# Performance work log

Measured on AMD Instinct MI355X. Metric: run time of the kernel, lower is better.

## Reference

```python
import jax, jax.numpy as jnp
import numpy as np

COMMITMENT_COST = 0.25


def setup_inputs() -> dict:
    key = jax.random.key(0)
    k1, k2 = jax.random.split(key)
    inputs = jax.random.normal(k1, (256, 512, 64), dtype=jnp.float32)
    embedding = jax.random.normal(k2, (1024, 64), dtype=jnp.float32) * 4.0
    return {"inputs": inputs, "embedding": embedding}


def reference(inputs, embedding):
    # inputs: [B, T, D], embedding: [K, D]
    input_shape = inputs.shape
    D = embedding.shape[-1]
    flat = inputs.reshape(-1, D)  # [N, D]
    # squared-L2 distances: [N, K]
    distances = (
        jnp.sum(flat * flat, axis=1, keepdims=True)
        + jnp.sum(embedding * embedding, axis=1)[None, :]
        - 2.0 * flat @ embedding.T
    )
    encoding_indices = jnp.argmin(distances, axis=1)  # [N]
    # one-hot @ embedding == gather
    quantized = embedding[encoding_indices].reshape(input_shape)  # [B, T, D]
    # squared-L2 commitment / codebook loss
    e_latent_loss = jnp.sum((jax.lax.stop_gradient(quantized) - inputs) ** 2, axis=-1)
    q_latent_loss = jnp.sum((quantized - jax.lax.stop_gradient(inputs)) ** 2, axis=-1)
    quantization_loss = q_latent_loss + COMMITMENT_COST * e_latent_loss  # [B, T]
    # straight-through estimator
    quantized_sg = inputs + jax.lax.stop_gradient(quantized - inputs)
    encoding_indices = encoding_indices.reshape(input_shape[:-1])  # [B, T]
    return quantized_sg, encoding_indices, quantization_loss
```

## Files before the change

### kernel.cpp

```cpp
#include <hip/hip_runtime.h>
#include <hip/hip_bf16.h>

#define D 64
#define KCODES 1024
#define MARGIN 0.25f
#define FLAG_CAP 8192

typedef __attribute__((ext_vector_type(8))) short bf16x8;
typedef __attribute__((ext_vector_type(4))) float f32x4;

__device__ inline unsigned short f2bf(float f) {
    union { __hip_bfloat16 h; unsigned short s; } cv;
    cv.h = __float2bfloat16(f);
    return cv.s;
}
__device__ inline float bf2f(unsigned short v) {
    union { unsigned short s; __hip_bfloat16 h; } cv;
    cv.s = v;
    return __bfloat162float(cv.h);
}

__global__ __launch_bounds__(256) void prep_kernel(
    const float* __restrict__ emb, float* __restrict__ e2,
    unsigned short* __restrict__ ehi, unsigned short* __restrict__ elo,
    unsigned int* __restrict__ counter) {
    int t = blockIdx.x * 256 + threadIdx.x;
    if (t == 0) *counter = 0u;
    if (t < KCODES) {
        const float4* ep = (const float4*)(emb + (size_t)t * D);
        float s0 = 0.f, s1 = 0.f, s2 = 0.f, s3 = 0.f;
#pragma unroll
        for (int i = 0; i < 16; ++i) {
            float4 v = ep[i];
            s0 = fmaf(v.x, v.x, s0);
            s1 = fmaf(v.y, v.y, s1);
            s2 = fmaf(v.z, v.z, s2);
            s3 = fmaf(v.w, v.w, s3);
        }
        e2[t] = (s0 + s1) + (s2 + s3);
    }
    float v = emb[t];
    unsigned short h = f2bf(v);
    ehi[t] = h;
    elo[t] = f2bf(v - bf2f(h));
}

__global__ __launch_bounds__(256) void vq_mfma_kernel(
    const float* __restrict__ x, const float* __restrict__ emb,
    const float* __restrict__ e2, const unsigned short* __restrict__ ehi,
    const unsigned short* __restrict__ elo, float* __restrict__ out_q,
    float* __restrict__ out_idx, float* __restrict__ out_loss,
    unsigned int* __restrict__ counter, int* __restrict__ flaglist) {
    __shared__ int s_bi[256];
    const int tid = threadIdx.x;
    const int lane = tid & 63;
    const int wave = __builtin_amdgcn_readfirstlane(tid >> 6);
    const int quad = lane >> 4;
    const int l15 = lane & 15;
    const int rowBase = blockIdx.x * 256 + wave * 64;

    bf16x8 ah[4][2], al[4][2];
#pragma unroll
    for (int rs = 0; rs < 4; ++rs) {
        const float* xr = x + (size_t)(rowBase + rs * 16 + l15) * D;
#pragma unroll
        for (int c = 0; c < 2; ++c) {
            const float4* p = (const float4*)(xr + c * 32 + quad * 8);
            float4 f0 = p[0], f1 = p[1];
            float f[8] = {f0.x, f0.y, f0.z, f0.w, f1.x, f1.y, f1.z, f1.w};
            bf16x8 h, l;
#pragma unroll
            for (int j = 0; j < 8; ++j) {
                unsigned short hu = f2bf(f[j]);
                h[j] = (short)hu;
                l[j] = (short)f2bf(f[j] - bf2f(hu));
            }
            ah[rs][c] = h;
            al[rs][c] = l;
        }
    }

    float m1[4][4], m2[4][4];
    int i1[4][4];
#pragma unroll
    for (int rs = 0; rs < 4; ++rs)
#pragma unroll
        for (int r = 0; r < 4; ++r) {
            m1[rs][r] = 3.4e38f;
            m2[rs][r] = 3.4e38f;
            i1[rs][r] = 0;
        }

    for (int t = 0; t < 64; ++t) {
        const int code = t * 16 + l15;
        const float e2v = e2[code];
        const unsigned short* hb = ehi + (size_t)code * D + quad * 8;
        const unsigned short* lb = elo + (size_t)code * D + quad * 8;
        bf16x8 bh0 = *(const bf16x8*)(hb);
        bf16x8 bh1 = *(const bf16x8*)(hb + 32);
        bf16x8 bl0 = *(const bf16x8*)(lb);
        bf16x8 bl1 = *(const bf16x8*)(lb + 32);
#pragma unroll
        for (int rs = 0; rs < 4; ++rs) {
            f32x4 acc = {0.f, 0.f, 0.f, 0.f};
            acc = __builtin_amdgcn_mfma_f32_16x16x32_bf16(ah[rs][0], bh0, acc, 0, 0, 0);
            acc = __builtin_amdgcn_mfma_f32_16x16x32_bf16(ah[rs][0], bl0, acc, 0, 0, 0);
            acc = __builtin_amdgcn_mfma_f32_16x16x32_bf16(al[rs][0], bh0, acc, 0, 0, 0);
            acc = __builtin_amdgcn_mfma_f32_16x16x32_bf16(ah[rs][1], bh1, acc, 0, 0, 0);
            acc = __builtin_amdgcn_mfma_f32_16x16x32_bf16(ah[rs][1], bl1, acc, 0, 0, 0);
            acc = __builtin_amdgcn_mfma_f32_16x16x32_bf16(al[rs][1], bh1, acc, 0, 0, 0);
#pragma unroll
            for (int r = 0; r < 4; ++r) {
                float v = fmaf(-2.0f, acc[r], e2v);
                if (v < m1[rs][r]) {
                    m2[rs][r] = m1[rs][r];
                    m1[rs][r] = v;
                    i1[rs][r] = code;
                } else {
                    m2[rs][r] = fminf(m2[rs][r], v);
                }
            }
        }
    }

#pragma unroll
    for (int rs = 0; rs < 4; ++rs)
#pragma unroll
        for (int r = 0; r < 4; ++r) {
            float v1 = m1[rs][r], v2 = m2[rs][r];
            int ix = i1[rs][r];
#pragma unroll
            for (int mask = 1; mask < 16; mask <<= 1) {
                float o1 = __shfl_xor(v1, mask);
                int oi = __shfl_xor(ix, mask);
                float o2 = __shfl_xor(v2, mask);
                v2 = fminf(fminf(v2, o2), fmaxf(v1, o1));
                bool take = (o1 < v1) || (o1 == v1 && oi < ix);
                v1 = take ? o1 : v1;
                ix = take ? oi : ix;
            }
            m1[rs][r] = v1;
            m2[rs][r] = v2;
            i1[rs][r] = ix;
        }

    if (l15 == 0) {
#pragma unroll
        for (int rs = 0; rs < 4; ++rs)
#pragma unroll
            for (int r = 0; r < 4; ++r) {
                int lrow = wave * 64 + rs * 16 + quad * 4 + r;
                s_bi[lrow] = i1[rs][r];
                if (m2[rs][r] - m1[rs][r] < MARGIN) {
                    unsigned int slot = atomicAdd(counter, 1u);
                    if (slot < FLAG_CAP) flaglist[slot] = blockIdx.x * 256 + lrow;
                }
            }
    }
    __syncthreads();

    {
        const int row = blockIdx.x * 256 + tid;
        const int bi = s_bi[tid];
        const float4* qp = (const float4*)(emb + (size_t)bi * D);
        const float4* xp = (const float4*)(x + (size_t)row * D);
        float4* oq = (float4*)(out_q + (size_t)row * D);
        float l0 = 0.f, l1 = 0.f, l2 = 0.f, l3 = 0.f;
#pragma unroll
        for (int i = 0; i < 16; ++i) {
            float4 q = qp[i];
            float4 xv = xp[i];
            float a0 = q.x - xv.x, a1 = q.y - xv.y, a2 = q.z - xv.z, a3 = q.w - xv.w;
            l0 = fmaf(a0, a0, l0);
            l1 = fmaf(a1, a1, l1);
            l2 = fmaf(a2, a2, l2);
            l3 = fmaf(a3, a3, l3);
            float4 o;
            o.x = xv.x + a0;
            o.y = xv.y + a1;
            o.z = xv.z + a2;
            o.w = xv.w + a3;
            oq[i] = o;
        }
        float s = (l0 + l1) + (l2 + l3);
        out_idx[row] = (float)bi;
        out_loss[row] = s + 0.25f * s;
    }
}

__global__ __launch_bounds__(256) void rescore_kernel(
    const float* __restrict__ x, const float* __restrict__ emb,
    const float* __restrict__ e2, float* __restrict__ out_q,
    float* __restrict__ out_idx, float* __restrict__ out_loss,
    const unsigned int* __restrict__ counter, const int* __restrict__ flaglist) {
    __shared__ float s_d[256];
    __shared__ int s_i[256];
    __shared__ float s_a[D];
    unsigned int n = *counter;
    if (n > FLAG_CAP) n = FLAG_CAP;
    const int tid = threadIdx.x;
    for (unsigned int f = blockIdx.x; f < n; f += gridDim.x) {
        const int row = flaglist[f];
        const float* xr = x + (size_t)row * D;
        float xv[D];
        const float4* xp = (const float4*)xr;
#pragma unroll
        for (int i = 0; i < 16; ++i) {
            float4 v = xp[i];
            xv[4 * i + 0] = v.x;
            xv[4 * i + 1] = v.y;
            xv[4 * i + 2] = v.z;
            xv[4 * i + 3] = v.w;
        }
        float bd = 3.4e38f;
        int bi = 0;
        for (int kk = 0; kk < 4; ++kk) {
            const int k = tid + kk * 256;
            const float* ek = emb + (size_t)k * D;
            float d0 = 0.f, d1 = 0.f, d2 = 0.f, d3 = 0.f;
#pragma unroll
            for (int i = 0; i < 16; ++i) {
                d0 = fmaf(xv[4 * i + 0], ek[4 * i + 0], d0);
                d1 = fmaf(xv[4 * i + 1], ek[4 * i + 1], d1);
                d2 = fmaf(xv[4 * i + 2], ek[4 * i + 2], d2);
                d3 = fmaf(xv[4 * i + 3], ek[4 * i + 3], d3);
            }
            float dist = fmaf(-2.0f, (d0 + d1) + (d2 + d3), e2[k]);
            if (dist < bd) { bd = dist; bi = k; }
        }
        s_d[tid] = bd;
        s_i[tid] = bi;
        __syncthreads();
        for (int s = 128; s > 0; s >>= 1) {
            if (tid < s) {
                float od = s_d[tid + s];
                int oi = s_i[tid + s];
                if (od < s_d[tid] || (od == s_d[tid] && oi < s_i[tid])) {
                    s_d[tid] = od;
                    s_i[tid] = oi;
                }
            }
            __syncthreads();
        }
        const int fbi = s_i[0];
        if (tid < D) {
            float xe = xr[tid];
            float a = emb[(size_t)fbi * D + tid] - xe;
            out_q[(size_t)row * D + tid] = xe + a;
            s_a[tid] = a * a;
        }
        __syncthreads();
        if (tid == 0) {
            float l0 = 0.f, l1 = 0.f, l2 = 0.f, l3 = 0.f;
            for (int i = 0; i < 16; ++i) {
                l0 += s_a[4 * i + 0];
                l1 += s_a[4 * i + 1];
                l2 += s_a[4 * i + 2];
                l3 += s_a[4 * i + 3];
            }
            float s = (l0 + l1) + (l2 + l3);
            out_loss[row] = s + 0.25f * s;
            out_idx[row] = (float)fbi;
        }
        __syncthreads();
    }
}

extern "C" void kernel_launch(void* const* d_in, const int* in_sizes, int n_in,
                              void* d_out, int out_size, void* d_ws, size_t ws_size,
                              hipStream_t stream) {
    const float* x = (const float*)d_in[0];
    const float* emb = (const float*)d_in[1];
    const int nrows = in_sizes[0] / D;

    float* out_q = (float*)d_out;
    float* out_idx = out_q + (size_t)nrows * D;
    float* out_loss = out_idx + nrows;

    char* ws = (char*)d_ws;
    float* e2 = (float*)ws;
    unsigned short* ehi = (unsigned short*)(ws + 4096);
    unsigned short* elo = (unsigned short*)(ws + 4096 + 131072);
    unsigned int* counter = (unsigned int*)(ws + 4096 + 2 * 131072);
    int* flaglist = (int*)(ws + 4096 + 2 * 131072 + 64);

    prep_kernel<<<(KCODES * D) / 256, 256, 0, stream>>>(emb, e2, ehi, elo, counter);
    vq_mfma_kernel<<<nrows / 256, 256, 0, stream>>>(x, emb, e2, ehi, elo, out_q,
                                                    out_idx, out_loss, counter,
                                                    flaglist);
    rescore_kernel<<<256, 256, 0, stream>>>(x, emb, e2, out_q, out_idx, out_loss,
                                            counter, flaglist);
}
```

Before: 195.1 us.

## Stage codebook through double-buffered LDS, pack argmin keys, batch rescore rows

The main kernel now handles 128 rows per block and stages the bf16 hi/lo codebook tiles through a double-buffered, XOR-swizzled LDS ring with explicit prefetch. It folds -2x into the bf16 split inputs and seeds the accumulator with an offset e2 so distances stay positive. That lets it pack the tile index into the low mantissa bits and track top-2 with v_med3_u32 and integer min. The rescore kernel processes 8 flagged rows per block, reusing each codebook load across them, and the flag capacity is derived from workspace size. Truncating mantissa bits and widening the margin to 0.6 trades argmin precision for fewer compare instructions but more rows sent to the rescore pass.

New measurement: 265.9 us. +36.3%, slower.

```diff
diff --git a/kernel.cpp b/kernel.cpp
--- a/kernel.cpp
+++ b/kernel.cpp
@@ -3,25 +3,25 @@
 
 #define D 64
 #define KCODES 1024
-#define MARGIN 0.25f
-#define FLAG_CAP 8192
+#define MARGIN 0.6f
+#define OFFSET 2048.0f
 
 typedef __attribute__((ext_vector_type(8))) short bf16x8;
 typedef __attribute__((ext_vector_type(4))) float f32x4;
 
-__device__ inline unsigned short f2bf(float f) {
+__device__ __forceinline__ unsigned short f2bf(float f) {
     union { __hip_bfloat16 h; unsigned short s; } cv;
     cv.h = __float2bfloat16(f);
     return cv.s;
 }
-__device__ inline float bf2f(unsigned short v) {
+__device__ __forceinline__ float bf2f(unsigned short v) {
     union { unsigned short s; __hip_bfloat16 h; } cv;
     cv.s = v;
     return __bfloat162float(cv.h);
 }
 
 __global__ __launch_bounds__(256) void prep_kernel(
-    const float* __restrict__ emb, float* __restrict__ e2,
+    const float* __restrict__ emb, float* __restrict__ e2, float* __restrict__ e2b,
     unsigned short* __restrict__ ehi, unsigned short* __restrict__ elo,
     unsigned int* __restrict__ counter) {
     int t = blockIdx.x * 256 + threadIdx.x;
@@ -37,7 +37,9 @@
             s2 = fmaf(v.z, v.z, s2);
             s3 = fmaf(v.w, v.w, s3);
         }
-        e2[t] = (s0 + s1) + (s2 + s3);
+        float s = (s0 + s1) + (s2 + s3);
+        e2[t] = s;
+        e2b[t] = s + OFFSET;
     }
     float v = emb[t];
     unsigned short h = f2bf(v);
@@ -45,23 +47,25 @@
     elo[t] = f2bf(v - bf2f(h));
 }
 
-__global__ __launch_bounds__(256) void vq_mfma_kernel(
+__global__ __launch_bounds__(256, 4) void vq_mfma_kernel(
     const float* __restrict__ x, const float* __restrict__ emb,
-    const float* __restrict__ e2, const unsigned short* __restrict__ ehi,
+    const float* __restrict__ e2b, const unsigned short* __restrict__ ehi,
     const unsigned short* __restrict__ elo, float* __restrict__ out_q,
     float* __restrict__ out_idx, float* __restrict__ out_loss,
-    unsigned int* __restrict__ counter, int* __restrict__ flaglist) {
-    __shared__ int s_bi[256];
+    unsigned int* __restrict__ counter, int* __restrict__ flaglist, int flag_cap) {
+    __shared__ float4 lds4[2][256];
+    __shared__ int s_bi[128];
+    char* ldsc = (char*)&lds4[0][0];
     const int tid = threadIdx.x;
     const int lane = tid & 63;
     const int wave = __builtin_amdgcn_readfirstlane(tid >> 6);
     const int quad = lane >> 4;
     const int l15 = lane & 15;
-    const int rowBase = blockIdx.x * 256 + wave * 64;
-
-    bf16x8 ah[4][2], al[4][2];
-#pragma unroll
-    for (int rs = 0; rs < 4; ++rs) {
+    const int rowBase = blockIdx.x * 128 + wave * 32;
+
+    bf16x8 ah[2][2], al[2][2];
+#pragma unroll
+    for (int rs = 0; rs < 2; ++rs) {
         const float* xr = x + (size_t)(rowBase + rs * 16 + l15) * D;
 #pragma unroll
         for (int c = 0; c < 2; ++c) {
@@ -71,96 +75,127 @@
             bf16x8 h, l;
 #pragma unroll
             for (int j = 0; j < 8; ++j) {
-                unsigned short hu = f2bf(f[j]);
+                float v = -2.0f * f[j];
+                unsigned short hu = f2bf(v);
                 h[j] = (short)hu;
-                l[j] = (short)f2bf(f[j] - bf2f(hu));
+                l[j] = (short)f2bf(v - bf2f(hu));
             }
             ah[rs][c] = h;
             al[rs][c] = l;
         }
     }
 
-    float m1[4][4], m2[4][4];
-    int i1[4][4];
-#pragma unroll
-    for (int rs = 0; rs < 4; ++rs)
+    const int r3 = lane >> 3;
+    const int sl = lane & 7;
+    const int halfsel = wave & 1;
+    const unsigned short* sbase = (wave < 2) ? ehi : elo;
+    const unsigned short* gsrc0 = sbase + halfsel * 512 + lane * 8;
+    const int wrow = halfsel * 8 + r3;
+    char* wdst = ldsc + ((wave < 2) ? 0 : 2048) + wrow * 128 + ((sl ^ r3) << 4);
+
+    const int s7 = l15 & 7;
+    const int rdA = l15 * 128 + ((quad ^ s7) << 4);
+    const int rdB = l15 * 128 + (((quad + 4) ^ s7) << 4);
+
+    unsigned int m1[2][4], m2[2][4];
+#pragma unroll
+    for (int rs = 0; rs < 2; ++rs)
+#pragma unroll
+        for (int r = 0; r < 4; ++r) { m1[rs][r] = 0xFFFFFFFFu; m2[rs][r] = 0xFFFFFFFFu; }
+
+    auto compute = [&](int t, float e2v, bf16x8 bh0, bf16x8 bh1, bf16x8 bl0, bf16x8 bl1) {
+        f32x4 cvec = {e2v, e2v, e2v, e2v};
+        unsigned tt = (unsigned)t;
+#pragma unroll
+        for (int rs = 0; rs < 2; ++rs) {
+            f32x4 acc = cvec;
+            acc = __builtin_amdgcn_mfma_f32_16x16x32_bf16(ah[rs][0], bh0, acc, 0, 0, 0);
+            acc = __builtin_amdgcn_mfma_f32_16x16x32_bf16(al[rs][0], bh0, acc, 0, 0, 0);
+            acc = __builtin_amdgcn_mfma_f32_16x16x32_bf16(ah[rs][0], bl0, acc, 0, 0, 0);
+            acc = __builtin_amdgcn_mfma_f32_16x16x32_bf16(ah[rs][1], bh1, acc, 0, 0, 0);
+            acc = __builtin_amdgcn_mfma_f32_16x16x32_bf16(al[rs][1], bh1, acc, 0, 0, 0);
+            acc = __builtin_amdgcn_mfma_f32_16x16x32_bf16(ah[rs][1], bl1, acc, 0, 0, 0);
+#pragma unroll
+            for (int r = 0; r < 4; ++r) {
+                unsigned k = (__float_as_uint(acc[r]) & 0xFFFFFFC0u) | tt;
+                unsigned nm2;
+                asm("v_med3_u32 %0, %1, %2, %3"
+                    : "=v"(nm2)
+                    : "v"(m1[rs][r]), "v"(m2[rs][r]), "v"(k));
+                m2[rs][r] = nm2;
+                m1[rs][r] = (k < m1[rs][r]) ? k : m1[rs][r];
+            }
+        }
+    };
+
+    float e2cur = e2b[l15];
+    {
+        float4 stg = *(const float4*)gsrc0;
+        *(float4*)wdst = stg;
+    }
+    __syncthreads();
+
+#pragma unroll 1
+    for (int i = 0; i < 32; ++i) {
+        const int tB = 2 * i + 1;
+        float4 stgB = *(const float4*)(gsrc0 + (size_t)tB * 1024);
+        float e2nA = e2b[tB * 16 + l15];
+        {
+            bf16x8 bh0 = *(const bf16x8*)(ldsc + rdA);
+            bf16x8 bh1 = *(const bf16x8*)(ldsc + rdB);
+            bf16x8 bl0 = *(const bf16x8*)(ldsc + 2048 + rdA);
+            bf16x8 bl1 = *(const bf16x8*)(ldsc + 2048 + rdB);
+            compute(2 * i, e2cur, bh0, bh1, bl0, bl1);
+        }
+        *(float4*)(wdst + 4096) = stgB;
+        __syncthreads();
+        float4 stgA2 = *(const float4*)(gsrc0 + (size_t)(tB + 1) * 1024);
+        float e2nB = e2b[(tB + 1) * 16 + l15];
+        {
+            bf16x8 bh0 = *(const bf16x8*)(ldsc + 4096 + rdA);
+            bf16x8 bh1 = *(const bf16x8*)(ldsc + 4096 + rdB);
+            bf16x8 bl0 = *(const bf16x8*)(ldsc + 6144 + rdA);
+            bf16x8 bl1 = *(const bf16x8*)(ldsc + 6144 + rdB);
+            compute(tB, e2nA, bh0, bh1, bl0, bl1);
+        }
+        *(float4*)wdst = stgA2;
+        __syncthreads();
+        e2cur = e2nB;
+    }
+
+#pragma unroll
+    for (int rs = 0; rs < 2; ++rs)
 #pragma unroll
         for (int r = 0; r < 4; ++r) {
-            m1[rs][r] = 3.4e38f;
-            m2[rs][r] = 3.4e38f;
-            i1[rs][r] = 0;
-        }
-
-    for (int t = 0; t < 64; ++t) {
-        const int code = t * 16 + l15;
-        const float e2v = e2[code];
-        const unsigned short* hb = ehi + (size_t)code * D + quad * 8;
-        const unsigned short* lb = elo + (size_t)code * D + quad * 8;
-        bf16x8 bh0 = *(const bf16x8*)(hb);
-        bf16x8 bh1 = *(const bf16x8*)(hb + 32);
-        bf16x8 bl0 = *(const bf16x8*)(lb);
-        bf16x8 bl1 = *(const bf16x8*)(lb + 32);
-#pragma unroll
-        for (int rs = 0; rs < 4; ++rs) {
-            f32x4 acc = {0.f, 0.f, 0.f, 0.f};
-            acc = __builtin_amdgcn_mfma_f32_16x16x32_bf16(ah[rs][0], bh0, acc, 0, 0, 0);
-            acc = __builtin_amdgcn_mfma_f32_16x16x32_bf16(ah[rs][0], bl0, acc, 0, 0, 0);
-            acc = __builtin_amdgcn_mfma_f32_16x16x32_bf16(al[rs][0], bh0, acc, 0, 0, 0);
-            acc = __builtin_amdgcn_mfma_f32_16x16x32_bf16(ah[rs][1], bh1, acc, 0, 0, 0);
-            acc = __builtin_amdgcn_mfma_f32_16x16x32_bf16(ah[rs][1], bl1, acc, 0, 0, 0);
-            acc = __builtin_amdgcn_mfma_f32_16x16x32_bf16(al[rs][1], bh1, acc, 0, 0, 0);
-#pragma unroll
-            for (int r = 0; r < 4; ++r) {
-                float v = fmaf(-2.0f, acc[r], e2v);
-                if (v < m1[rs][r]) {
-                    m2[rs][r] = m1[rs][r];
-                    m1[rs][r] = v;
-                    i1[rs][r] = code;
-                } else {
-                    m2[rs][r] = fminf(m2[rs][r], v);
+            unsigned v1 = m1[rs][r], v2 = m2[rs][r];
+            const unsigned my1 = v1;
+#pragma unroll
+            for (int mask = 1; mask < 16; mask <<= 1) {
+                unsigned o1 = __shfl_xor(v1, mask);
+                unsigned o2 = __shfl_xor(v2, mask);
+                unsigned hi = v1 > o1 ? v1 : o1;
+                unsigned lo2 = v2 < o2 ? v2 : o2;
+                v2 = lo2 < hi ? lo2 : hi;
+                v1 = v1 < o1 ? v1 : o1;
+            }
+            unsigned long long bal = __ballot(my1 == v1);
+            int winl = __ffsll((bal >> (quad * 16)) & 0xFFFFull) - 1;
+            int code = (int)(v1 & 63u) * 16 + winl;
+            if (l15 == 0) {
+                int lrow = wave * 32 + rs * 16 + quad * 4 + r;
+                s_bi[lrow] = code;
+                float f1 = __uint_as_float(v1 & 0xFFFFFFC0u);
+                float f2 = __uint_as_float(v2 & 0xFFFFFFC0u);
+                if (f2 - f1 < MARGIN) {
+                    unsigned slot = atomicAdd(counter, 1u);
+                    if (slot < (unsigned)flag_cap) flaglist[slot] = blockIdx.x * 128 + lrow;
                 }
             }
         }
-    }
-
-#pragma unroll
-    for (int rs = 0; rs < 4; ++rs)
-#pragma unroll
-        for (int r = 0; r < 4; ++r) {
-            float v1 = m1[rs][r], v2 = m2[rs][r];
-            int ix = i1[rs][r];
-#pragma unroll
-            for (int mask = 1; mask < 16; mask <<= 1) {
-                float o1 = __shfl_xor(v1, mask);
-                int oi = __shfl_xor(ix, mask);
-                float o2 = __shfl_xor(v2, mask);
-                v2 = fminf(fminf(v2, o2), fmaxf(v1, o1));
-                bool take = (o1 < v1) || (o1 == v1 && oi < ix);
-                v1 = take ? o1 : v1;
-                ix = take ? oi : ix;
-            }
-            m1[rs][r] = v1;
-            m2[rs][r] = v2;
-            i1[rs][r] = ix;
-        }
-
-    if (l15 == 0) {
-#pragma unroll
-        for (int rs = 0; rs < 4; ++rs)
-#pragma unroll
-            for (int r = 0; r < 4; ++r) {
-                int lrow = wave * 64 + rs * 16 + quad * 4 + r;
-                s_bi[lrow] = i1[rs][r];
-                if (m2[rs][r] - m1[rs][r] < MARGIN) {
-                    unsigned int slot = atomicAdd(counter, 1u);
-                    if (slot < FLAG_CAP) flaglist[slot] = blockIdx.x * 256 + lrow;
-                }
-            }
-    }
     __syncthreads();
 
-    {
-        const int row = blockIdx.x * 256 + tid;
+    if (tid < 128) {
+        const int row = blockIdx.x * 128 + tid;
         const int bi = s_bi[tid];
         const float4* qp = (const float4*)(emb + (size_t)bi * D);
         const float4* xp = (const float4*)(x + (size_t)row * D);
@@ -192,77 +227,113 @@
     const float* __restrict__ x, const float* __restrict__ emb,
     const float* __restrict__ e2, float* __restrict__ out_q,
     float* __restrict__ out_idx, float* __restrict__ out_loss,
-    const unsigned int* __restrict__ counter, const int* __restrict__ flaglist) {
-    __shared__ float s_d[256];
-    __shared__ int s_i[256];
-    __shared__ float s_a[D];
+    const unsigned int* __restrict__ counter, const int* __restrict__ flaglist,
+    int flag_cap) {
+    __shared__ float s_x[8][64];
+    __shared__ int s_rows[8];
+    __shared__ float s_wd[8][4];
+    __shared__ int s_wi[8][4];
+    __shared__ float s_a[4][64];
     unsigned int n = *counter;
-    if (n > FLAG_CAP) n = FLAG_CAP;
+    if (n > (unsigned)flag_cap) n = (unsigned)flag_cap;
     const int tid = threadIdx.x;
-    for (unsigned int f = blockIdx.x; f < n; f += gridDim.x) {
-        const int row = flaglist[f];
-        const float* xr = x + (size_t)row * D;
-        float xv[D];
-        const float4* xp = (const float4*)xr;
-#pragma unroll
-        for (int i = 0; i < 16; ++i) {
-            float4 v = xp[i];
-            xv[4 * i + 0] = v.x;
-            xv[4 * i + 1] = v.y;
-            xv[4 * i + 2] = v.z;
-            xv[4 * i + 3] = v.w;
-        }
-        float bd = 3.4e38f;
-        int bi = 0;
+    const int lane = tid & 63;
+    const int wv = tid >> 6;
+    for (unsigned int b = blockIdx.x; b * 8u < n; b += gridDim.x) {
+        const unsigned base = b * 8u;
+        unsigned nbu = n - base;
+        if (nbu > 8u) nbu = 8u;
+        const int nb = (int)nbu;
+        if (tid < 8) s_rows[tid] = flaglist[base + (tid < nb ? tid : 0)];
+        __syncthreads();
+        if (tid < 128) {
+            int r = tid >> 4, q4 = tid & 15;
+            ((float4*)&s_x[r][0])[q4] = ((const float4*)(x + (size_t)s_rows[r] * D))[q4];
+        }
+        __syncthreads();
+
+        float bd_[8];
+        int bi_[8];
+#pragma unroll
+        for (int r = 0; r < 8; ++r) { bd_[r] = 3.4e38f; bi_[r] = 0; }
         for (int kk = 0; kk < 4; ++kk) {
             const int k = tid + kk * 256;
             const float* ek = emb + (size_t)k * D;
-            float d0 = 0.f, d1 = 0.f, d2 = 0.f, d3 = 0.f;
+            float d0[8], d1[8], d2[8], d3[8];
+#pragma unroll
+            for (int r = 0; r < 8; ++r) { d0[r] = 0.f; d1[r] = 0.f; d2[r] = 0.f; d3[r] = 0.f; }
 #pragma unroll
             for (int i = 0; i < 16; ++i) {
-                d0 = fmaf(xv[4 * i + 0], ek[4 * i + 0], d0);
-                d1 = fmaf(xv[4 * i + 1], ek[4 * i + 1], d1);
-                d2 = fmaf(xv[4 * i + 2], ek[4 * i + 2], d2);
-                d3 = fmaf(xv[4 * i + 3], ek[4 * i + 3], d3);
-            }
-            float dist = fmaf(-2.0f, (d0 + d1) + (d2 + d3), e2[k]);
-            if (dist < bd) { bd = dist; bi = k; }
-        }
-        s_d[tid] = bd;
-        s_i[tid] = bi;
-        __syncthreads();
-        for (int s = 128; s > 0; s >>= 1) {
-            if (tid < s) {
-                float od = s_d[tid + s];
-                int oi = s_i[tid + s];
-                if (od < s_d[tid] || (od == s_d[tid] && oi < s_i[tid])) {
-                    s_d[tid] = od;
-                    s_i[tid] = oi;
+                float4 ev = ((const float4*)ek)[i];
+#pragma unroll
+                for (int r = 0; r < 8; ++r) {
+                    float4 xv = ((const float4*)&s_x[r][0])[i];
+                    d0[r] = fmaf(xv.x, ev.x, d0[r]);
+                    d1[r] = fmaf(xv.y, ev.y, d1[r]);
+                    d2[r] = fmaf(xv.z, ev.z, d2[r]);
+                    d3[r] = fmaf(xv.w, ev.w, d3[r]);
                 }
             }
+            float e2k = e2[k];
+#pragma unroll
+            for (int r = 0; r < 8; ++r) {
+                float dist = fmaf(-2.0f, (d0[r] + d1[r]) + (d2[r] + d3[r]), e2k);
+                if (dist < bd_[r]) { bd_[r] = dist; bi_[r] = k; }
+            }
+        }
+#pragma unroll
+        for (int r = 0; r < 8; ++r) {
+            float v = bd_[r];
+            int ix = bi_[r];
+#pragma unroll
+            for (int mask = 1; mask < 64; mask <<= 1) {
+                float ov = __shfl_xor(v, mask);
+                int oi = __shfl_xor(ix, mask);
+                bool tk = (ov < v) || (ov == v && oi < ix);
+                v = tk ? ov : v;
+                ix = tk ? oi : ix;
+            }
+            if (lane == 0) { s_wd[r][wv] = v; s_wi[r][wv] = ix; }
+        }
+        __syncthreads();
+        if (tid < 8) {
+            float v = s_wd[tid][0];
+            int ix = s_wi[tid][0];
+#pragma unroll
+            for (int w = 1; w < 4; ++w) {
+                float ov = s_wd[tid][w];
+                int oi = s_wi[tid][w];
+                bool tk = (ov < v) || (ov == v && oi < ix);
+                v = tk ? ov : v;
+                ix = tk ? oi : ix;
+            }
+            s_wi[tid][0] = ix;
+        }
+        __syncthreads();
+#pragma unroll
+        for (int pass = 0; pass < 2; ++pass) {
+            const int rloc = pass * 4 + wv;
+            const int row = s_rows[rloc];
+            const int fbi = s_wi[rloc][0];
+            const float xe = s_x[rloc][lane];
+            const float a = emb[(size_t)fbi * D + lane] - xe;
+            if (rloc < nb) out_q[(size_t)row * D + lane] = xe + a;
+            s_a[wv][lane] = a * a;
             __syncthreads();
-        }
-        const int fbi = s_i[0];
-        if (tid < D) {
-            float xe = xr[tid];
-            float a = emb[(size_t)fbi * D + tid] - xe;
-            out_q[(size_t)row * D + tid] = xe + a;
-            s_a[tid] = a * a;
-        }
-        __syncthreads();
-        if (tid == 0) {
-            float l0 = 0.f, l1 = 0.f, l2 = 0.f, l3 = 0.f;
-            for (int i = 0; i < 16; ++i) {
-                l0 += s_a[4 * i + 0];
-                l1 += s_a[4 * i + 1];
-                l2 += s_a[4 * i + 2];
-                l3 += s_a[4 * i + 3];
-            }
-            float s = (l0 + l1) + (l2 + l3);
-            out_loss[row] = s + 0.25f * s;
-            out_idx[row] = (float)fbi;
-        }
-        __syncthreads();
+            if (lane == 0 && rloc < nb) {
+                float l0 = 0.f, l1 = 0.f, l2 = 0.f, l3 = 0.f;
+                for (int i2 = 0; i2 < 16; ++i2) {
+                    l0 += s_a[wv][4 * i2 + 0];
+                    l1 += s_a[wv][4 * i2 + 1];
+                    l2 += s_a[wv][4 * i2 + 2];
+                    l3 += s_a[wv][4 * i2 + 3];
+                }
+                float s = (l0 + l1) + (l2 + l3);
+                out_loss[row] = s + 0.25f * s;
+                out_idx[row] = (float)fbi;
+            }
+            __syncthreads();
+        }
     }
 }
 
@@ -279,15 +350,20 @@
 
     char* ws = (char*)d_ws;
     float* e2 = (float*)ws;
-    unsigned short* ehi = (unsigned short*)(ws + 4096);
-    unsigned short* elo = (unsigned short*)(ws + 4096 + 131072);
-    unsigned int* counter = (unsigned int*)(ws + 4096 + 2 * 131072);
-    int* flaglist = (int*)(ws + 4096 + 2 * 131072 + 64);
-
-    prep_kernel<<<(KCODES * D) / 256, 256, 0, stream>>>(emb, e2, ehi, elo, counter);
-    vq_mfma_kernel<<<nrows / 256, 256, 0, stream>>>(x, emb, e2, ehi, elo, out_q,
+    float* e2b = (float*)(ws + 4096);
+    unsigned short* ehi = (unsigned short*)(ws + 8192);
+    unsigned short* elo = (unsigned short*)(ws + 8192 + 131072);
+    unsigned int* counter = (unsigned int*)(ws + 8192 + 262144);
+    int* flaglist = (int*)(ws + 8192 + 262144 + 64);
+    long long avail = (long long)ws_size - (8192 + 262144 + 64);
+    int flag_cap = (int)(avail / 4);
+    if (flag_cap > 16384) flag_cap = 16384;
+    if (flag_cap < 1024) flag_cap = 1024;
+
+    prep_kernel<<<(KCODES * D) / 256, 256, 0, stream>>>(emb, e2, e2b, ehi, elo, counter);
+    vq_mfma_kernel<<<nrows / 128, 256, 0, stream>>>(x, emb, e2b, ehi, elo, out_q,
                                                     out_idx, out_loss, counter,
-                                                    flaglist);
-    rescore_kernel<<<256, 256, 0, stream>>>(x, emb, e2, out_q, out_idx, out_loss,
-                                            counter, flaglist);
-}
+                                                    flaglist, flag_cap);
+    rescore_kernel<<<1024, 256, 0, stream>>>(x, emb, e2, out_q, out_idx, out_loss,
+                                             counter, flaglist, flag_cap);
+}
```
